# Kernel tuning notes

Measured on AMD Instinct MI355X. Metric: run time of the kernel, lower is better.

## Reference

```python
import jax, jax.numpy as jnp
import numpy as np

N_NODES = 16384
FM = 256
N_EDGES = 524288


def gcn_conv(x, W, b, edge_index, edge_weight):
    """PyG GCNConv: y = D^-1/2 (A+I) D^-1/2 (x @ W) + b, with edge weights."""
    n = x.shape[0]
    loop = jnp.arange(n)
    src = jnp.concatenate([edge_index[0], loop])
    dst = jnp.concatenate([edge_index[1], loop])
    w = jnp.concatenate([edge_weight, jnp.ones((n,), edge_weight.dtype)])
    deg = jax.ops.segment_sum(w, dst, num_segments=n)
    dinv = jnp.where(deg > 0, jax.lax.rsqrt(jnp.maximum(deg, 1e-30)), 0.0)
    norm = dinv[src] * w * dinv[dst]            # [E+n]
    h = x @ W                                    # [n, fm]
    msg = h[src] * norm[:, None]                 # [E+n, fm] gather
    return jax.ops.segment_sum(msg, dst, num_segments=n) + b


def setup_inputs() -> dict:
    key = jax.random.key(0)
    ks = jax.random.split(key, 24)
    inp = {
        "x": jax.random.normal(ks[0], (N_NODES, FM), jnp.float32),
        "edges_f": jax.random.randint(ks[1], (2, N_EDGES), 0, N_NODES),
        "ew_f": jax.random.uniform(ks[2], (N_EDGES,), jnp.float32),
        "edges_s": jax.random.randint(ks[3], (2, N_EDGES), 0, N_NODES),
        "ew_s": jax.random.uniform(ks[4], (N_EDGES,), jnp.float32),
        "edges_g": jax.random.randint(ks[5], (2, N_EDGES), 0, N_NODES),
        "ew_g": jax.random.uniform(ks[6], (N_EDGES,), jnp.float32),
    }
    names = ["f1", "f2", "s1", "s2", "g1", "g2"]
    for i, nm in enumerate(names):
        inp["W" + nm] = 0.05 * jax.random.normal(ks[7 + i], (FM, FM), jnp.float32)
        inp["b" + nm] = jnp.zeros((FM,), jnp.float32)
    inp["fc1_w"] = 0.5 * jax.random.normal(ks[13], (30, 6), jnp.float32)
    inp["fc1_b"] = jnp.zeros((30,), jnp.float32)
    inp["fc2_w"] = 0.5 * jax.random.normal(ks[14], (6, 30), jnp.float32)
    inp["fc2_b"] = jnp.zeros((6,), jnp.float32)
    inp["cnn_w"] = 0.5 * jax.random.normal(ks[15], (6,), jnp.float32)
    inp["cnn_b"] = jnp.zeros((1,), jnp.float32)
    return inp


def reference(x, edges_f, ew_f, edges_s, ew_s, edges_g, ew_g,
              Wf1, bf1, Wf2, bf2, Ws1, bs1, Ws2, bs2, Wg1, bg1, Wg2, bg2,
              fc1_w, fc1_b, fc2_w, fc2_b, cnn_w, cnn_b):
    # three 2-layer GCN branches with relu
    f1 = jax.nn.relu(gcn_conv(x, Wf1, bf1, edges_f, ew_f))
    f2 = jax.nn.relu(gcn_conv(f1, Wf2, bf2, edges_f, ew_f))
    s1 = jax.nn.relu(gcn_conv(x, Ws1, bs1, edges_s, ew_s))
    s2 = jax.nn.relu(gcn_conv(s1, Ws2, bs2, edges_s, ew_s))
    g1 = jax.nn.relu(gcn_conv(x, Wg1, bg1, edges_g, ew_g))
    g2 = jax.nn.relu(gcn_conv(g1, Wg2, bg2, edges_g, ew_g))
    # cat along features then t().view(1,6,fm,N) == stack of transposed branches
    XM = jnp.stack([f1.T, f2.T, s1.T, s2.T, g1.T, g2.T])  # [6, fm, N]
    # SE channel attention
    pooled = jnp.mean(XM, axis=(1, 2))                     # [6]
    h = jax.nn.relu(fc1_w @ pooled + fc1_b)                # [30]
    att = jax.nn.sigmoid(fc2_w @ h + fc2_b)                # [6]
    XM_att = jax.nn.relu(att[:, None, None] * XM)          # [6, fm, N]
    # 1x1 conv 6->1 channels
    out = jnp.einsum('c,cfn->fn', cnn_w, XM_att) + cnn_b[0]  # [fm, N]
    return out.T                                            # [N, fm]
```

## Files before the change

kernel.cpp:

```cpp
#include <hip/hip_runtime.h>
#include <hip/hip_bf16.h>

#define N_NODES 16384
#define FM      256
#define NF      (N_NODES * FM)
#define NF4     (NF / 4)

typedef __attribute__((ext_vector_type(8))) short short8;
typedef __attribute__((ext_vector_type(4))) float f32x4;

__device__ inline ushort f2bf(float f) {
    uint u = __float_as_uint(f);
    return (ushort)((u + 0x7FFFu + ((u >> 16) & 1u)) >> 16);
}
__device__ inline uint pack2bf(float a, float b) {
    return (uint)f2bf(a) | ((uint)f2bf(b) << 16);
}
__device__ inline float bf2f(ushort u) { return __uint_as_float(((uint)u) << 16); }

__global__ void init_kernel(float* __restrict__ dinv3, int* __restrict__ cnt3,
                            float* __restrict__ pooled) {
    int i = blockIdx.x * blockDim.x + threadIdx.x;
    int n3 = 3 * N_NODES;
    if (i < n3) {
        dinv3[i] = 1.0f;
        cnt3[i] = 0;
    } else if (i < n3 + 6) {
        pooled[i - n3] = 0.0f;
    }
}

__global__ void deg_edges_all(const int* __restrict__ d0, const int* __restrict__ d1,
                              const int* __restrict__ d2,
                              const float* __restrict__ e0, const float* __restrict__ e1,
                              const float* __restrict__ e2,
                              float* __restrict__ deg3, int* __restrict__ cnt3, int E) {
    int t = blockIdx.y;
    const int* dst = (t == 0) ? d0 : (t == 1) ? d1 : d2;
    const float* ew = (t == 0) ? e0 : (t == 1) ? e1 : e2;
    float* deg = deg3 + t * N_NODES;
    int* cnt = cnt3 + t * N_NODES;
    int e = blockIdx.x * blockDim.x + threadIdx.x;
    if (e < E) {
        int d = dst[e];
        atomicAdd(&deg[d], ew[e]);
        atomicAdd(&cnt[d], 1);
    }
}

__global__ void deg_finish_kernel(float* __restrict__ deg, int n3) {
    int i = blockIdx.x * blockDim.x + threadIdx.x;
    if (i < n3) deg[i] = rsqrtf(deg[i]);
}

__global__ __launch_bounds__(1024) void scan_all(const int* __restrict__ cnt3,
                                                 int* __restrict__ rowstart3,
                                                 int* __restrict__ cursor3) {
    const int* cnt = cnt3 + blockIdx.x * N_NODES;
    int* row_start = rowstart3 + blockIdx.x * (N_NODES + 2);
    int* cursor = cursor3 + blockIdx.x * N_NODES;
    __shared__ int part[1024];
    int t = threadIdx.x;
    int base = t * 16;
    int local[16];
    int s = 0;
#pragma unroll
    for (int i = 0; i < 16; ++i) { local[i] = cnt[base + i]; s += local[i]; }
    part[t] = s;
    __syncthreads();
    for (int off = 1; off < 1024; off <<= 1) {
        int v = (t >= off) ? part[t - off] : 0;
        __syncthreads();
        part[t] += v;
        __syncthreads();
    }
    int pre = (t > 0) ? part[t - 1] : 0;
#pragma unroll
    for (int i = 0; i < 16; ++i) {
        row_start[base + i] = pre;
        cursor[base + i] = pre;
        pre += local[i];
    }
    if (t == 1023) row_start[N_NODES] = pre;
}

__global__ void scatter_all(const int* __restrict__ s0, const int* __restrict__ s1,
                            const int* __restrict__ s2,
                            const float* __restrict__ e0, const float* __restrict__ e1,
                            const float* __restrict__ e2,
                            const float* __restrict__ dinv3,
                            int* __restrict__ cursor3,
                            int* __restrict__ csrsrc3, float* __restrict__ csrnorm3,
                            int E) {
    int t = blockIdx.y;
    const int* ed = (t == 0) ? s0 : (t == 1) ? s1 : s2;
    const float* ew = (t == 0) ? e0 : (t == 1) ? e1 : e2;
    const float* dinv = dinv3 + t * N_NODES;
    int* cursor = cursor3 + t * N_NODES;
    int* csr_src = csrsrc3 + (size_t)t * E;
    float* csr_norm = csrnorm3 + (size_t)t * E;
    int e = blockIdx.x * blockDim.x + threadIdx.x;
    if (e >= E) return;
    int s = ed[e], d = ed[E + e];
    int pos = atomicAdd(&cursor[d], 1);
    csr_src[pos] = s;
    csr_norm[pos] = dinv[s] * ew[e] * dinv[d];
}

__global__ __launch_bounds__(256) void wpack_kernel(const float* __restrict__ w0,
                                                    const float* __restrict__ w1,
                                                    const float* __restrict__ w2,
                                                    const float* __restrict__ w3,
                                                    const float* __restrict__ w4,
                                                    const float* __restrict__ w5,
                                                    ushort* __restrict__ wt) {
    const float* W;
    switch (blockIdx.z) {
        case 0: W = w0; break; case 1: W = w1; break; case 2: W = w2; break;
        case 3: W = w3; break; case 4: W = w4; break; default: W = w5; break;
    }
    __shared__ float tl[16][17];
    int tx = threadIdx.x & 15, ty = threadIdx.x >> 4;
    int k0 = blockIdx.x * 16, n0 = blockIdx.y * 16;
    tl[ty][tx] = W[(size_t)(k0 + ty) * FM + n0 + tx];
    __syncthreads();
    wt[(size_t)blockIdx.z * FM * FM + (size_t)(n0 + ty) * FM + k0 + tx] = f2bf(tl[tx][ty]);
}

__global__ __launch_bounds__(256) void gemm_mfma(const float* __restrict__ A,
                                                 const ushort* __restrict__ WT,
                                                 ushort* __restrict__ C) {
    __shared__ ushort A_lds[128 * 64];

    const int tid = threadIdx.x;
    const int lane = tid & 63;
    const int wid = tid >> 6;
    const int wm = wid >> 1, wn = wid & 1;
    const int bm = blockIdx.x * 128;
    const int bn = blockIdx.y * 64;

    const int l15 = lane & 15;
    const int lg = lane >> 4;

    f32x4 acc[4][2];
#pragma unroll
    for (int i = 0; i < 4; ++i)
#pragma unroll
        for (int n = 0; n < 2; ++n) acc[i][n] = (f32x4){0.f, 0.f, 0.f, 0.f};

    const int srow = tid >> 1;
    const int shk = tid & 1;
    const float* arow_p = &A[(size_t)(bm + srow) * FM + shk * 32];

    for (int k0 = 0; k0 < 256; k0 += 64) {
        {
            const float* ap = arow_p + k0;
#pragma unroll
            for (int g = 0; g < 4; ++g) {
                float4 a0 = *(const float4*)(ap + g * 8);
                float4 a1 = *(const float4*)(ap + g * 8 + 4);
                uint4 pk;
                pk.x = pack2bf(a0.x, a0.y);
                pk.y = pack2bf(a0.z, a0.w);
                pk.z = pack2bf(a1.x, a1.y);
                pk.w = pack2bf(a1.z, a1.w);
                int kk = shk * 32 + g * 8;
                int idx = srow * 64 + (kk ^ ((srow & 7) << 3));
                *(uint4*)&A_lds[idx] = pk;
            }
        }
        __syncthreads();
#pragma unroll
        for (int s = 0; s < 2; ++s) {
            short8 bfrag[2];
#pragma unroll
            for (int n = 0; n < 2; ++n) {
                int col = bn + wn * 32 + n * 16 + l15;
                bfrag[n] = *(const short8*)&WT[(size_t)col * FM + k0 + s * 32 + lg * 8];
            }
#pragma unroll
            for (int i = 0; i < 4; ++i) {
                int row = wm * 64 + i * 16 + l15;
                int kk = s * 32 + lg * 8;
                short8 afrag = *(const short8*)&A_lds[row * 64 + (kk ^ ((row & 7) << 3))];
#pragma unroll
                for (int n = 0; n < 2; ++n)
                    acc[i][n] = __builtin_amdgcn_mfma_f32_16x16x32_bf16(
                        afrag, bfrag[n], acc[i][n], 0, 0, 0);
            }
        }
        __syncthreads();
    }
#pragma unroll
    for (int i = 0; i < 4; ++i) {
#pragma unroll
        for (int n = 0; n < 2; ++n) {
            int col = bn + wn * 32 + n * 16 + l15;
#pragma unroll
            for (int r = 0; r < 4; ++r) {
                int row = bm + wm * 64 + i * 16 + lg * 4 + r;
                C[(size_t)row * FM + col] = f2bf(acc[i][n][r]);
            }
        }
    }
}

__global__ __launch_bounds__(256) void gcn_aggregate_csr(const ushort* __restrict__ h,
                                                         const int* __restrict__ row_start,
                                                         const int* __restrict__ csr_src,
                                                         const float* __restrict__ csr_norm,
                                                         const float* __restrict__ dinv,
                                                         const float* __restrict__ bias,
                                                         float* __restrict__ out) {
    int node = blockIdx.x * 4 + (threadIdx.x >> 6);
    int lane = threadIdx.x & 63;
    const ushort4* hp = (const ushort4*)h;

    float di = dinv[node];
    float sw = di * di;
    ushort4 q = hp[(size_t)node * 64 + lane];
    float4 accA = make_float4(bf2f(q.x) * sw, bf2f(q.y) * sw,
                              bf2f(q.z) * sw, bf2f(q.w) * sw);
    float4 accB = make_float4(0.f, 0.f, 0.f, 0.f);

    int beg = row_start[node];
    int end = row_start[node + 1];
    int j = beg;
    for (; j + 3 < end; j += 4) {
        int s0 = csr_src[j];
        int s1 = csr_src[j + 1];
        int s2 = csr_src[j + 2];
        int s3 = csr_src[j + 3];
        float w0 = csr_norm[j];
        float w1 = csr_norm[j + 1];
        float w2 = csr_norm[j + 2];
        float w3 = csr_norm[j + 3];
        ushort4 q0 = hp[(size_t)s0 * 64 + lane];
        ushort4 q1 = hp[(size_t)s1 * 64 + lane];
        ushort4 q2 = hp[(size_t)s2 * 64 + lane];
        ushort4 q3 = hp[(size_t)s3 * 64 + lane];
        accA.x += w0 * bf2f(q0.x) + w1 * bf2f(q1.x);
        accA.y += w0 * bf2f(q0.y) + w1 * bf2f(q1.y);
        accA.z += w0 * bf2f(q0.z) + w1 * bf2f(q1.z);
        accA.w += w0 * bf2f(q0.w) + w1 * bf2f(q1.w);
        accB.x += w2 * bf2f(q2.x) + w3 * bf2f(q3.x);
        accB.y += w2 * bf2f(q2.y) + w3 * bf2f(q3.y);
        accB.z += w2 * bf2f(q2.z) + w3 * bf2f(q3.z);
        accB.w += w2 * bf2f(q2.w) + w3 * bf2f(q3.w);
    }
    for (; j < end; ++j) {
        int s0 = csr_src[j];
        float w0 = csr_norm[j];
        ushort4 q0 = hp[(size_t)s0 * 64 + lane];
        accA.x += w0 * bf2f(q0.x);
        accA.y += w0 * bf2f(q0.y);
        accA.z += w0 * bf2f(q0.z);
        accA.w += w0 * bf2f(q0.w);
    }
    float4 bb = ((const float4*)bias)[lane];
    float4 acc;
    acc.x = fmaxf(accA.x + accB.x + bb.x, 0.0f);
    acc.y = fmaxf(accA.y + accB.y + bb.y, 0.0f);
    acc.z = fmaxf(accA.z + accB.z + bb.z, 0.0f);
    acc.w = fmaxf(accA.w + accB.w + bb.w, 0.0f);
    ((float4*)out)[(size_t)node * 64 + lane] = acc;
}

__global__ __launch_bounds__(256) void reduce_branch_kernel(const float* __restrict__ br,
                                                            float* __restrict__ pooled) {
    int c = blockIdx.y;
    const float4* p = (const float4*)(br + (size_t)c * NF + (size_t)blockIdx.x * 16384);
    float s = 0.0f;
#pragma unroll
    for (int i = 0; i < 16; ++i) {
        float4 v = p[threadIdx.x + i * 256];
        s += v.x + v.y + v.z + v.w;
    }
    for (int o = 32; o > 0; o >>= 1) s += __shfl_down(s, o);
    __shared__ float wsum[4];
    if ((threadIdx.x & 63) == 0) wsum[threadIdx.x >> 6] = s;
    __syncthreads();
    if (threadIdx.x == 0)
        atomicAdd(&pooled[c], wsum[0] + wsum[1] + wsum[2] + wsum[3]);
}

__global__ void se_kernel(const float* __restrict__ pooled_sum,
                          const float* __restrict__ fc1_w, const float* __restrict__ fc1_b,
                          const float* __restrict__ fc2_w, const float* __restrict__ fc2_b,
                          float* __restrict__ att) {
    __shared__ float p[6];
    __shared__ float hbuf[30];
    int t = threadIdx.x;
    if (t < 6) p[t] = pooled_sum[t] * (1.0f / ((float)N_NODES * (float)FM));
    __syncthreads();
    if (t < 30) {
        float a = fc1_b[t];
#pragma unroll
        for (int c = 0; c < 6; ++c) a += fc1_w[t * 6 + c] * p[c];
        hbuf[t] = fmaxf(a, 0.0f);
    }
    __syncthreads();
    if (t < 6) {
        float a = fc2_b[t];
#pragma unroll
        for (int j = 0; j < 30; ++j) a += fc2_w[t * 30 + j] * hbuf[j];
        att[t] = 1.0f / (1.0f + expf(-a));
    }
}

__global__ void combine_kernel(const float* __restrict__ br,
                               const float* __restrict__ att,
                               const float* __restrict__ cnn_w,
                               const float* __restrict__ cnn_b,
                               float* __restrict__ out, int total4) {
    int i = blockIdx.x * blockDim.x + threadIdx.x;
    if (i >= total4) return;
    float a[6], w[6];
#pragma unroll
    for (int c = 0; c < 6; ++c) { a[c] = att[c]; w[c] = cnn_w[c]; }
    float cb = cnn_b[0];
    float4 acc = make_float4(cb, cb, cb, cb);
#pragma unroll
    for (int c = 0; c < 6; ++c) {
        float4 v = ((const float4*)(br + (size_t)c * NF))[i];
        acc.x += w[c] * fmaxf(a[c] * v.x, 0.0f);
        acc.y += w[c] * fmaxf(a[c] * v.y, 0.0f);
        acc.z += w[c] * fmaxf(a[c] * v.z, 0.0f);
        acc.w += w[c] * fmaxf(a[c] * v.w, 0.0f);
    }
    ((float4*)out)[i] = acc;
}


static void run_conv(const float* in, const ushort* wtp, const float* b,
                     const int* row_start, const int* csr_src, const float* csr_norm,
                     const float* dinv, ushort* h_bf16, float* out,
                     hipStream_t stream) {
    dim3 ggrid(N_NODES / 128, FM / 64);
    gemm_mfma<<<ggrid, 256, 0, stream>>>(in, wtp, h_bf16);
    gcn_aggregate_csr<<<N_NODES / 4, 256, 0, stream>>>(h_bf16, row_start, csr_src,
                                                       csr_norm, dinv, b, out);
}

extern "C" void kernel_launch(void* const* d_in, const int* in_sizes, int n_in,
                              void* d_out, int out_size, void* d_ws, size_t ws_size,
                              hipStream_t stream) {
    const float* x      = (const float*)d_in[0];
    const int*   ed_f   = (const int*)d_in[1];
    const float* ew_f   = (const float*)d_in[2];
    const int*   ed_s   = (const int*)d_in[3];
    const float* ew_s   = (const float*)d_in[4];
    const int*   ed_g   = (const int*)d_in[5];
    const float* ew_g   = (const float*)d_in[6];
    const float* Wf1 = (const float*)d_in[7];  const float* bf1 = (const float*)d_in[8];
    const float* Wf2 = (const float*)d_in[9];  const float* bf2 = (const float*)d_in[10];
    const float* Ws1 = (const float*)d_in[11]; const float* bs1 = (const float*)d_in[12];
    const float* Ws2 = (const float*)d_in[13]; const float* bs2 = (const float*)d_in[14];
    const float* Wg1 = (const float*)d_in[15]; const float* bg1 = (const float*)d_in[16];
    const float* Wg2 = (const float*)d_in[17]; const float* bg2 = (const float*)d_in[18];
    const float* fc1_w = (const float*)d_in[19]; const float* fc1_b = (const float*)d_in[20];
    const float* fc2_w = (const float*)d_in[21]; const float* fc2_b = (const float*)d_in[22];
    const float* cnn_w = (const float*)d_in[23]; const float* cnn_b = (const float*)d_in[24];

    const int E = in_sizes[1] / 2;

    float* ws = (float*)d_ws;
    float* br = ws;
    float* dinv3  = ws + (size_t)6 * NF;
    float* pooled = dinv3 + 3 * N_NODES;
    float* att    = pooled + 6;
    int*   cnt3      = (int*)(att + 10);
    int*   cursor3   = cnt3 + 3 * N_NODES;
    int*   rowstart3 = cursor3 + 3 * N_NODES;
    int*   csr_src3  = rowstart3 + 3 * (N_NODES + 2);
    float* csr_norm3 = (float*)(csr_src3 + (size_t)3 * E);
    ushort* wt       = (ushort*)(csr_norm3 + (size_t)3 * E);

    float* dinv_set[3] = { dinv3, dinv3 + N_NODES, dinv3 + 2 * N_NODES };
    int*   rs_set[3]   = { rowstart3, rowstart3 + (N_NODES + 2),
                           rowstart3 + 2 * (N_NODES + 2) };
    int*   csrc_set[3] = { csr_src3, csr_src3 + E, csr_src3 + 2 * E };
    float* cnorm_set[3] = { csr_norm3, csr_norm3 + E, csr_norm3 + 2 * E };

    float* f1 = br + (size_t)0 * NF;
    float* f2 = br + (size_t)1 * NF;
    float* s1 = br + (size_t)2 * NF;
    float* s2 = br + (size_t)3 * NF;
    float* g1 = br + (size_t)4 * NF;
    float* g2 = br + (size_t)5 * NF;

    ushort* h = (ushort*)d_out;

    int n3 = 3 * N_NODES;
    init_kernel<<<(n3 + 6 + 255) / 256, 256, 0, stream>>>(dinv3, cnt3, pooled);
    {
        dim3 dg((E + 255) / 256, 3);
        deg_edges_all<<<dg, 256, 0, stream>>>(ed_f + E, ed_s + E, ed_g + E,
                                              ew_f, ew_s, ew_g, dinv3, cnt3, E);
    }
    deg_finish_kernel<<<(n3 + 255) / 256, 256, 0, stream>>>(dinv3, n3);
    scan_all<<<3, 1024, 0, stream>>>(cnt3, rowstart3, cursor3);
    {
        dim3 sg((E + 255) / 256, 3);
        scatter_all<<<sg, 256, 0, stream>>>(ed_f, ed_s, ed_g, ew_f, ew_s, ew_g,
                                            dinv3, cursor3, csr_src3, csr_norm3, E);
    }
    {
        dim3 wg(16, 16, 6);
        wpack_kernel<<<wg, 256, 0, stream>>>(Wf1, Wf2, Ws1, Ws2, Wg1, Wg2, wt);
    }
    const ushort* wt_set[6] = { wt, wt + 65536, wt + 2 * 65536,
                                wt + 3 * 65536, wt + 4 * 65536, wt + 5 * 65536 };

    run_conv(x,  wt_set[0], bf1, rs_set[0], csrc_set[0], cnorm_set[0], dinv_set[0], h, f1, stream);
    run_conv(f1, wt_set[1], bf2, rs_set[0], csrc_set[0], cnorm_set[0], dinv_set[0], h, f2, stream);
    run_conv(x,  wt_set[2], bs1, rs_set[1], csrc_set[1], cnorm_set[1], dinv_set[1], h, s1, stream);
    run_conv(s1, wt_set[3], bs2, rs_set[1], csrc_set[1], cnorm_set[1], dinv_set[1], h, s2, stream);
    run_conv(x,  wt_set[4], bg1, rs_set[2], csrc_set[2], cnorm_set[2], dinv_set[2], h, g1, stream);
    run_conv(g1, wt_set[5], bg2, rs_set[2], csrc_set[2], cnorm_set[2], dinv_set[2], h, g2, stream);

    dim3 rgrid(256, 6);
    reduce_branch_kernel<<<rgrid, 256, 0, stream>>>(br, pooled);
    se_kernel<<<1, 64, 0, stream>>>(pooled, fc1_w, fc1_b, fc2_w, fc2_b, att);

    combine_kernel<<<NF4 / 256, 256, 0, stream>>>(br, att, cnn_w, cnn_b,
                                                  (float*)d_out, NF4);
}
```

Baseline: 608.5 us.

## Partition CSR build across 8 counter copies and compute degrees from CSR

Edge counting and scatter now use 8 partitioned counter arrays, chosen by block index, to spread atomic contention. Float degree atomics are replaced by a per-node reduction over the built CSR. A second scan produces node-level offsets, and a compaction kernel merges the partitions into the final CSR with precomputed norms. This adds several kernels, a larger serial 131K-element scan in 3 blocks, and extra memory passes, in exchange for less atomic contention.

```diff
diff --git a/kernel.cpp b/kernel.cpp
--- a/kernel.cpp
+++ b/kernel.cpp
@@ -5,8 +5,13 @@
 #define FM      256
 #define NF      (N_NODES * FM)
 #define NF4     (NF / 4)
+#define NPART   8
+#define NSCAN   (NPART * N_NODES)
+#define RS_STRIDE 131076
+#define NRS_STRIDE (N_NODES + 2)
 
 typedef __attribute__((ext_vector_type(8))) short short8;
+typedef __attribute__((ext_vector_type(8))) ushort ushort8;
 typedef __attribute__((ext_vector_type(4))) float f32x4;
 
 __device__ inline ushort f2bf(float f) {
@@ -18,54 +23,35 @@
 }
 __device__ inline float bf2f(ushort u) { return __uint_as_float(((uint)u) << 16); }
 
-__global__ void init_kernel(float* __restrict__ dinv3, int* __restrict__ cnt3,
-                            float* __restrict__ pooled) {
+__global__ void init_kernel(int* __restrict__ cnt3, float* __restrict__ pooled) {
     int i = blockIdx.x * blockDim.x + threadIdx.x;
-    int n3 = 3 * N_NODES;
-    if (i < n3) {
-        dinv3[i] = 1.0f;
-        cnt3[i] = 0;
-    } else if (i < n3 + 6) {
-        pooled[i - n3] = 0.0f;
-    }
-}
-
-__global__ void deg_edges_all(const int* __restrict__ d0, const int* __restrict__ d1,
+    int n = 3 * NSCAN;
+    if (i < n) cnt3[i] = 0;
+    else if (i < n + 6) pooled[i - n] = 0.0f;
+}
+
+__global__ void cnt_edges_all(const int* __restrict__ d0, const int* __restrict__ d1,
                               const int* __restrict__ d2,
-                              const float* __restrict__ e0, const float* __restrict__ e1,
-                              const float* __restrict__ e2,
-                              float* __restrict__ deg3, int* __restrict__ cnt3, int E) {
+                              int* __restrict__ cnt3, int E) {
     int t = blockIdx.y;
     const int* dst = (t == 0) ? d0 : (t == 1) ? d1 : d2;
-    const float* ew = (t == 0) ? e0 : (t == 1) ? e1 : e2;
-    float* deg = deg3 + t * N_NODES;
-    int* cnt = cnt3 + t * N_NODES;
+    int part = blockIdx.x & (NPART - 1);
+    int* cnt = cnt3 + t * NSCAN + part * N_NODES;
     int e = blockIdx.x * blockDim.x + threadIdx.x;
-    if (e < E) {
-        int d = dst[e];
-        atomicAdd(&deg[d], ew[e]);
-        atomicAdd(&cnt[d], 1);
-    }
-}
-
-__global__ void deg_finish_kernel(float* __restrict__ deg, int n3) {
-    int i = blockIdx.x * blockDim.x + threadIdx.x;
-    if (i < n3) deg[i] = rsqrtf(deg[i]);
+    if (e < E) atomicAdd(&cnt[dst[e]], 1);
 }
 
 __global__ __launch_bounds__(1024) void scan_all(const int* __restrict__ cnt3,
                                                  int* __restrict__ rowstart3,
                                                  int* __restrict__ cursor3) {
-    const int* cnt = cnt3 + blockIdx.x * N_NODES;
-    int* row_start = rowstart3 + blockIdx.x * (N_NODES + 2);
-    int* cursor = cursor3 + blockIdx.x * N_NODES;
+    const int* cnt = cnt3 + blockIdx.x * NSCAN;
+    int* row_start = rowstart3 + blockIdx.x * RS_STRIDE;
+    int* cursor = cursor3 + blockIdx.x * NSCAN;
     __shared__ int part[1024];
     int t = threadIdx.x;
-    int base = t * 16;
-    int local[16];
+    int base = t * 128;
     int s = 0;
-#pragma unroll
-    for (int i = 0; i < 16; ++i) { local[i] = cnt[base + i]; s += local[i]; }
+    for (int i = 0; i < 128; ++i) s += cnt[base + i];
     part[t] = s;
     __syncthreads();
     for (int off = 1; off < 1024; off <<= 1) {
@@ -75,36 +61,114 @@
         __syncthreads();
     }
     int pre = (t > 0) ? part[t - 1] : 0;
-#pragma unroll
-    for (int i = 0; i < 16; ++i) {
+    for (int i = 0; i < 128; ++i) {
+        int c = cnt[base + i];
         row_start[base + i] = pre;
         cursor[base + i] = pre;
+        pre += c;
+    }
+    if (t == 1023) row_start[NSCAN] = pre;
+}
+
+__global__ __launch_bounds__(1024) void scan_nodes(const int* __restrict__ cnt3,
+                                                   int* __restrict__ nodestart3) {
+    const int* cnt = cnt3 + blockIdx.x * NSCAN;
+    int* nrs = nodestart3 + blockIdx.x * NRS_STRIDE;
+    __shared__ int part[1024];
+    int t = threadIdx.x;
+    int base = t * 16;
+    int local[16];
+    int s = 0;
+#pragma unroll
+    for (int i = 0; i < 16; ++i) {
+        int tot = 0;
+#pragma unroll
+        for (int p = 0; p < NPART; ++p) tot += cnt[p * N_NODES + base + i];
+        local[i] = tot;
+        s += tot;
+    }
+    part[t] = s;
+    __syncthreads();
+    for (int off = 1; off < 1024; off <<= 1) {
+        int v = (t >= off) ? part[t - off] : 0;
+        __syncthreads();
+        part[t] += v;
+        __syncthreads();
+    }
+    int pre = (t > 0) ? part[t - 1] : 0;
+#pragma unroll
+    for (int i = 0; i < 16; ++i) {
+        nrs[base + i] = pre;
         pre += local[i];
     }
-    if (t == 1023) row_start[N_NODES] = pre;
+    if (t == 1023) nrs[N_NODES] = pre;
 }
 
 __global__ void scatter_all(const int* __restrict__ s0, const int* __restrict__ s1,
                             const int* __restrict__ s2,
                             const float* __restrict__ e0, const float* __restrict__ e1,
                             const float* __restrict__ e2,
-                            const float* __restrict__ dinv3,
-                            int* __restrict__ cursor3,
-                            int* __restrict__ csrsrc3, float* __restrict__ csrnorm3,
-                            int E) {
+                            int* __restrict__ cursor3, int2* __restrict__ csr3, int E) {
     int t = blockIdx.y;
     const int* ed = (t == 0) ? s0 : (t == 1) ? s1 : s2;
     const float* ew = (t == 0) ? e0 : (t == 1) ? e1 : e2;
-    const float* dinv = dinv3 + t * N_NODES;
-    int* cursor = cursor3 + t * N_NODES;
-    int* csr_src = csrsrc3 + (size_t)t * E;
-    float* csr_norm = csrnorm3 + (size_t)t * E;
+    int part = blockIdx.x & (NPART - 1);
+    int* cursor = cursor3 + t * NSCAN + part * N_NODES;
+    int2* csr = csr3 + (size_t)t * E;
     int e = blockIdx.x * blockDim.x + threadIdx.x;
     if (e >= E) return;
     int s = ed[e], d = ed[E + e];
     int pos = atomicAdd(&cursor[d], 1);
-    csr_src[pos] = s;
-    csr_norm[pos] = dinv[s] * ew[e] * dinv[d];
+    csr[pos] = make_int2(s, __float_as_int(ew[e]));
+}
+
+__global__ __launch_bounds__(256) void deg_dinv_all(const int2* __restrict__ csr3,
+                                                    const int* __restrict__ rowstart3,
+                                                    float* __restrict__ dinv3, int E) {
+    int t = blockIdx.y;
+    const int2* csr = csr3 + (size_t)t * E;
+    const int* rs = rowstart3 + t * RS_STRIDE;
+    int node = blockIdx.x * 4 + (threadIdx.x >> 6);
+    int lane = threadIdx.x & 63;
+    int p = lane >> 3;
+    int l8 = lane & 7;
+    int beg = rs[p * N_NODES + node], end = rs[p * N_NODES + node + 1];
+    float s = 0.0f;
+    for (int j = beg + l8; j < end; j += 8)
+        s += __int_as_float(csr[j].y);
+    for (int o = 32; o > 0; o >>= 1) s += __shfl_down(s, o);
+    if (lane == 0) dinv3[t * N_NODES + node] = rsqrtf(1.0f + s);
+}
+
+__global__ __launch_bounds__(256) void compact_norm_all(const int2* __restrict__ csr3,
+                                                        const int* __restrict__ rowstart3,
+                                                        const int* __restrict__ nodestart3,
+                                                        const float* __restrict__ dinv3,
+                                                        int* __restrict__ csrsrc3,
+                                                        float* __restrict__ csrnorm3,
+                                                        int E) {
+    int t = blockIdx.y;
+    const int2* src = csr3 + (size_t)t * E;
+    const int* prs = rowstart3 + t * RS_STRIDE;
+    const int* nrs = nodestart3 + t * NRS_STRIDE;
+    const float* dinv = dinv3 + t * N_NODES;
+    int* dsrc = csrsrc3 + (size_t)t * E;
+    float* dnorm = csrnorm3 + (size_t)t * E;
+    int node = blockIdx.x * 4 + (threadIdx.x >> 6);
+    int lane = threadIdx.x & 63;
+    float din = dinv[node];
+    int w = nrs[node];
+#pragma unroll
+    for (int p = 0; p < NPART; ++p) {
+        int beg = prs[p * N_NODES + node];
+        int end = prs[p * N_NODES + node + 1];
+        for (int j = beg + lane; j < end; j += 64) {
+            int2 c = src[j];
+            dsrc[w + (j - beg)] = c.x;
+            dnorm[w + (j - beg)] = __int_as_float(c.y) * dinv[c.x] * din;
+        }
+        w += end - beg;
+    }
 }
 
 __global__ __launch_bounds__(256) void wpack_kernel(const float* __restrict__ w0,
@@ -138,7 +202,6 @@
     const int wm = wid >> 1, wn = wid & 1;
     const int bm = blockIdx.x * 128;
     const int bn = blockIdx.y * 64;
-
     const int l15 = lane & 15;
     const int lg = lane >> 4;
 
@@ -368,17 +431,19 @@
     float* br = ws;
     float* dinv3  = ws + (size_t)6 * NF;
     float* pooled = dinv3 + 3 * N_NODES;
-    float* att    = pooled + 6;
-    int*   cnt3      = (int*)(att + 10);
-    int*   cursor3   = cnt3 + 3 * N_NODES;
-    int*   rowstart3 = cursor3 + 3 * N_NODES;
-    int*   csr_src3  = rowstart3 + 3 * (N_NODES + 2);
-    float* csr_norm3 = (float*)(csr_src3 + (size_t)3 * E);
-    ushort* wt       = (ushort*)(csr_norm3 + (size_t)3 * E);
+    float* att    = pooled + 8;
+    int*   cnt3       = (int*)(att + 8);
+    int*   cursor3    = cnt3 + 3 * NSCAN;
+    int*   rowstart3  = cursor3 + 3 * NSCAN;
+    int*   nodestart3 = rowstart3 + 3 * RS_STRIDE;
+    int2*  csr3       = (int2*)(nodestart3 + 3 * NRS_STRIDE + 2);
+    int*   csr_src3   = (int*)(csr3 + (size_t)3 * E);
+    float* csr_norm3  = (float*)(csr_src3 + (size_t)3 * E);
+    ushort* wt        = (ushort*)(csr_norm3 + (size_t)3 * E);
 
     float* dinv_set[3] = { dinv3, dinv3 + N_NODES, dinv3 + 2 * N_NODES };
-    int*   rs_set[3]   = { rowstart3, rowstart3 + (N_NODES + 2),
-                           rowstart3 + 2 * (N_NODES + 2) };
+    int*   nrs_set[3]  = { nodestart3, nodestart3 + NRS_STRIDE,
+                           nodestart3 + 2 * NRS_STRIDE };
     int*   csrc_set[3] = { csr_src3, csr_src3 + E, csr_src3 + 2 * E };
     float* cnorm_set[3] = { csr_norm3, csr_norm3 + E, csr_norm3 + 2 * E };
 
@@ -391,19 +456,26 @@
 
     ushort* h = (ushort*)d_out;
 
-    int n3 = 3 * N_NODES;
-    init_kernel<<<(n3 + 6 + 255) / 256, 256, 0, stream>>>(dinv3, cnt3, pooled);
+    init_kernel<<<(3 * NSCAN + 6 + 255) / 256, 256, 0, stream>>>(cnt3, pooled);
     {
-        dim3 dg((E + 255) / 256, 3);
-        deg_edges_all<<<dg, 256, 0, stream>>>(ed_f + E, ed_s + E, ed_g + E,
-                                              ew_f, ew_s, ew_g, dinv3, cnt3, E);
-    }
-    deg_finish_kernel<<<(n3 + 255) / 256, 256, 0, stream>>>(dinv3, n3);
+        dim3 g((E + 255) / 256, 3);
+        cnt_edges_all<<<g, 256, 0, stream>>>(ed_f + E, ed_s + E, ed_g + E, cnt3, E);
+    }
     scan_all<<<3, 1024, 0, stream>>>(cnt3, rowstart3, cursor3);
+    scan_nodes<<<3, 1024, 0, stream>>>(cnt3, nodestart3);
     {
-        dim3 sg((E + 255) / 256, 3);
-        scatter_all<<<sg, 256, 0, stream>>>(ed_f, ed_s, ed_g, ew_f, ew_s, ew_g,
-                                            dinv3, cursor3, csr_src3, csr_norm3, E);
+        dim3 g((E + 255) / 256, 3);
+        scatter_all<<<g, 256, 0, stream>>>(ed_f, ed_s, ed_g, ew_f, ew_s, ew_g,
+                                           cursor3, csr3, E);
+    }
+    {
+        dim3 g(N_NODES / 4, 3);
+        deg_dinv_all<<<g, 256, 0, stream>>>(csr3, rowstart3, dinv3, E);
+    }
+    {
+        dim3 g(N_NODES / 4, 3);
+        compact_norm_all<<<g, 256, 0, stream>>>(csr3, rowstart3, nodestart3, dinv3,
+                                                csr_src3, csr_norm3, E);
     }
     {
         dim3 wg(16, 16, 6);
@@ -412,12 +484,12 @@
     const ushort* wt_set[6] = { wt, wt + 65536, wt + 2 * 65536,
                                 wt + 3 * 65536, wt + 4 * 65536, wt + 5 * 65536 };
 
-    run_conv(x,  wt_set[0], bf1, rs_set[0], csrc_set[0], cnorm_set[0], dinv_set[0], h, f1, stream);
-    run_conv(f1, wt_set[1], bf2, rs_set[0], csrc_set[0], cnorm_set[0], dinv_set[0], h, f2, stream);
-    run_conv(x,  wt_set[2], bs1, rs_set[1], csrc_set[1], cnorm_set[1], dinv_set[1], h, s1, stream);
-    run_conv(s1, wt_set[3], bs2, rs_set[1], csrc_set[1], cnorm_set[1], dinv_set[1], h, s2, stream);
-    run_conv(x,  wt_set[4], bg1, rs_set[2], csrc_set[2], cnorm_set[2], dinv_set[2], h, g1, stream);
-    run_conv(g1, wt_set[5], bg2, rs_set[2], csrc_set[2], cnorm_set[2], dinv_set[2], h, g2, stream);
+    run_conv(x,  wt_set[0], bf1, nrs_set[0], csrc_set[0], cnorm_set[0], dinv_set[0], h, f1, stream);
+    run_conv(f1, wt_set[1], bf2, nrs_set[0], csrc_set[0], cnorm_set[0], dinv_set[0], h, f2, stream);
+    run_conv(x,  wt_set[2], bs1, nrs_set[1], csrc_set[1], cnorm_set[1], dinv_set[1], h, s1, stream);
+    run_conv(s1, wt_set[3], bs2, nrs_set[1], csrc_set[1], cnorm_set[1], dinv_set[1], h, s2, stream);
+    run_conv(x,  wt_set[4], bg1, nrs_set[2], csrc_set[2], cnorm_set[2], dinv_set[2], h, g1, stream);
+    run_conv(g1, wt_set[5], bg2, nrs_set[2], csrc_set[2], cnorm_set[2], dinv_set[2], h, g2, stream);
 
     dim3 rgrid(256, 6);
     reduce_branch_kernel<<<rgrid, 256, 0, stream>>>(br, pooled);
```

Result: slower. 641.8 us (+5.5%).
